# Kernel optimization log

Hardware: AMD Instinct MI355X
Metric: run time of the kernel (lower is better)

Reference implementation:

```python
import jax, jax.numpy as jnp
import numpy as np

H = 8          # num_heads
D = 256        # num_hiddens (left == right embed dim)
DH = D // H    # per-head dim
SH = 64        # num_attention_score_hiddens
B = 4
L_LEFT = 128
L_RIGHT = 256
NEG = -1e6


def _split_heads(x):
    # [B, L, D] -> [B*H, L, D/H]
    b, l, d = x.shape
    return x.reshape(b, l, H, d // H).transpose(0, 2, 1, 3).reshape(b * H, l, d // H)


def _merge_heads(x):
    # [B*H, L, dh] -> [B, L, H*dh]
    bh, l, dh = x.shape
    return x.reshape(-1, H, l, dh).transpose(0, 2, 1, 3).reshape(-1, l, H * dh)


def _additive_attention(q, k, v, valid, Wq, Wk, wv):
    # q: [BH, Lq, dh], k/v: [BH, Lk, dh], valid: [BH] int
    qf = q @ Wq                                   # [BH, Lq, SH]
    kf = k @ Wk                                   # [BH, Lk, SH]
    feats = jnp.tanh(qf[:, :, None, :] + kf[:, None, :, :])   # [BH, Lq, Lk, SH]
    scores = jnp.einsum('bqkh,h->bqk', feats, wv)              # [BH, Lq, Lk]
    lk = k.shape[1]
    mask = jnp.arange(lk)[None, None, :] < valid[:, None, None]
    scores = jnp.where(mask, scores, NEG)
    w = jax.nn.softmax(scores, axis=-1)
    return w @ v                                  # [BH, Lq, dh]


def setup_inputs() -> dict:
    key = jax.random.key(0)
    ks = jax.random.split(key, 16)
    f32 = jnp.float32
    s_w = 1.0 / np.sqrt(DH)
    s_v = 1.0 / np.sqrt(SH)
    s_o = 1.0 / np.sqrt(D)
    return {
        'queries_left': jax.random.normal(ks[0], (B, L_LEFT, D), f32),
        'keys_right':   jax.random.normal(ks[1], (B, L_RIGHT, D), f32),
        'values_right': jax.random.normal(ks[2], (B, L_RIGHT, D), f32),
        'queries_right': jax.random.normal(ks[3], (B, L_RIGHT, D), f32),
        'keys_left':    jax.random.normal(ks[4], (B, L_LEFT, D), f32),
        'values_left':  jax.random.normal(ks[5], (B, L_LEFT, D), f32),
        'Wq_l': jax.random.normal(ks[6], (DH, SH), f32) * s_w,
        'Wk_l': jax.random.normal(ks[7], (DH, SH), f32) * s_w,
        'wv_l': jax.random.normal(ks[8], (SH,), f32) * s_v,
        'Wo_l': jax.random.normal(ks[9], (D, D), f32) * s_o,
        'Wq_r': jax.random.normal(ks[10], (DH, SH), f32) * s_w,
        'Wk_r': jax.random.normal(ks[11], (DH, SH), f32) * s_w,
        'wv_r': jax.random.normal(ks[12], (SH,), f32) * s_v,
        'Wo_r': jax.random.normal(ks[13], (D, D), f32) * s_o,
        'valid_lens_right': jax.random.randint(ks[14], (B,), 1, L_RIGHT + 1).astype(jnp.int32),
        'valid_lens_left':  jax.random.randint(ks[15], (B,), 1, L_LEFT + 1).astype(jnp.int32),
    }


def reference(queries_left, keys_right, values_right, queries_right, keys_left,
              values_left, Wq_l, Wk_l, wv_l, Wo_l, Wq_r, Wk_r, wv_r, Wo_r,
              valid_lens_right, valid_lens_left):
    ql = _split_heads(queries_left)
    kr = _split_heads(keys_right)
    vr = _split_heads(values_right)
    qr = _split_heads(queries_right)
    kl = _split_heads(keys_left)
    vl = _split_heads(values_left)
    vlr = jnp.repeat(valid_lens_right, H)   # [B*H]
    vll = jnp.repeat(valid_lens_left, H)
    out_l = _additive_attention(ql, kr, vr, vlr, Wq_l, Wk_l, wv_l)
    out_r = _additive_attention(qr, kl, vl, vll, Wq_r, Wk_r, wv_r)
    out_l = _merge_heads(out_l) @ Wo_l      # [B, L_LEFT, D]
    out_r = _merge_heads(out_r) @ Wo_r      # [B, L_RIGHT, D]
    return out_l, out_r
```

## Files before the change

### kernel.cpp

```cpp
#include <hip/hip_runtime.h>
#include <math.h>


#define LOG2E 1.4426950408889634f
#define SCALE2 (2.0f * LOG2E)
#define NEGS  (-2.0f * LOG2E)

#define OFF_EQL 0
#define OFF_EKL 262144
#define OFF_EQR 786432
#define OFF_EKR 1310720
#define OFF_PL  1572864
#define OFF_PR  2621440
#define OFF_HOL 3670016
#define OFF_HOR 3801088

static __device__ __forceinline__ float fast_exp2(float x) {
#if __has_builtin(__builtin_amdgcn_exp2f)
    return __builtin_amdgcn_exp2f(x);
#else
    return exp2f(x);
#endif
}
static __device__ __forceinline__ float fast_rcp(float x) {
#if __has_builtin(__builtin_amdgcn_rcpf)
    return __builtin_amdgcn_rcpf(x);
#else
    return 1.0f / x;
#endif
}

__global__ __launch_bounds__(256) void k1_proj(
    const float* __restrict__ ql, const float* __restrict__ kr,
    const float* __restrict__ qr, const float* __restrict__ kl,
    const float* __restrict__ wql, const float* __restrict__ wkl,
    const float* __restrict__ wqr, const float* __restrict__ wkr,
    float* __restrict__ ws)
{
    __shared__ float tlds[64 * 17];
    int blk = blockIdx.x;
    const float* X; const float* W; float* out; int L; int ktype;
    if (blk < 256)       { X = ql; W = wql; out = ws + OFF_EQL; L = 128; ktype = 0; }
    else if (blk < 768)  { X = kr; W = wkl; out = ws + OFF_EKL; L = 256; ktype = 1; blk -= 256; }
    else if (blk < 1280) { X = qr; W = wqr; out = ws + OFF_EQR; L = 256; ktype = 0; blk -= 768; }
    else                 { X = kl; W = wkr; out = ws + OFF_EKR; L = 128; ktype = 1; blk -= 1280; }

    const int tiles = L >> 4;
    const int bh = blk / tiles;
    const int l0 = (blk - bh * tiles) << 4;
    const int b = bh >> 3, hd = bh & 7;
    const int t = threadIdx.x;
    const int h = t & 63, lsub = t >> 6;

    float wcol[32];
#pragma unroll
    for (int j = 0; j < 32; ++j) wcol[j] = W[j * 64 + h];

    const float* xb = X + ((b * L + l0 + lsub * 4) * 256) + hd * 32;

#pragma unroll
    for (int i = 0; i < 4; ++i) {
        const float4* xp = (const float4*)(xb + i * 256);
        float acc = 0.f;
#pragma unroll
        for (int j4 = 0; j4 < 8; ++j4) {
            float4 a = xp[j4];
            acc += a.x * wcol[4 * j4 + 0];
            acc += a.y * wcol[4 * j4 + 1];
            acc += a.z * wcol[4 * j4 + 2];
            acc += a.w * wcol[4 * j4 + 3];
        }
        const float e = fast_exp2(acc * SCALE2);
        const int lloc = lsub * 4 + i;
        if (!ktype) out[(bh * L + l0 + lloc) * 64 + h] = e;
        else        tlds[h * 17 + lloc] = e;
    }
    if (ktype) {
        __syncthreads();
        const int ll = t & 15, hq = t >> 4;
#pragma unroll
        for (int hh = 0; hh < 4; ++hh) {
            const int h2 = hq + 16 * hh;
            out[bh * (64 * L) + h2 * L + l0 + ll] = tlds[h2 * 17 + ll];
        }
    }
}

template<int LK, int LQ, int RPT, int J>
static __device__ __forceinline__ void scores_side(
    int bh, int row0,
    const float* __restrict__ eq, const float* __restrict__ ek,
    const float* __restrict__ wv, int valid, float* __restrict__ P)
{
    const int lane = threadIdx.x & 63;
    float acc[RPT][J];
#pragma unroll
    for (int r = 0; r < RPT; ++r)
#pragma unroll
        for (int j = 0; j < J; ++j) acc[r][j] = 0.f;

    const float* ekb = ek + bh * (64 * LK) + lane;
    const float* eqb = eq + (bh * LQ + row0) * 64;

#pragma unroll
    for (int j = 0; j < J; ++j) {
        if (64 * j < valid) {
#pragma unroll
            for (int hc = 0; hc < 16; ++hc) {
                const float4 wv4 = *(const float4*)(wv + hc * 4);
                float wva[4] = {wv4.x, wv4.y, wv4.z, wv4.w};
                float eqa[RPT][4];
#pragma unroll
                for (int r = 0; r < RPT; ++r) {
                    const float4 q4 = *(const float4*)(eqb + r * 64 + hc * 4);
                    eqa[r][0] = q4.x; eqa[r][1] = q4.y; eqa[r][2] = q4.z; eqa[r][3] = q4.w;
                }
#pragma unroll
                for (int hs = 0; hs < 4; ++hs) {
                    const float ekv = ekb[(hc * 4 + hs) * LK + 64 * j];
#pragma unroll
                    for (int pr = 0; pr < RPT / 2; ++pr) {
                        const float d0 = fmaf(eqa[2 * pr    ][hs], ekv, 1.0f);
                        const float d1 = fmaf(eqa[2 * pr + 1][hs], ekv, 1.0f);
                        const float rr = fast_rcp(d0 * d1);
                        acc[2 * pr    ][j] += (wva[hs] * d1) * rr;
                        acc[2 * pr + 1][j] += (wva[hs] * d0) * rr;
                    }
                }
            }
        }
    }

#pragma unroll
    for (int r = 0; r < RPT; ++r) {
        float sv[J];
        float m = -3.0e38f;
#pragma unroll
        for (int j = 0; j < J; ++j) {
            sv[j] = (64 * j + lane < valid) ? acc[r][j] * NEGS : -1.0e6f;
            m = fmaxf(m, sv[j]);
        }
#pragma unroll
        for (int off = 1; off < 64; off <<= 1) m = fmaxf(m, __shfl_xor(m, off));
        float lsum = 0.f;
#pragma unroll
        for (int j = 0; j < J; ++j) { sv[j] = fast_exp2(sv[j] - m); lsum += sv[j]; }
#pragma unroll
        for (int off = 1; off < 64; off <<= 1) lsum += __shfl_xor(lsum, off);
        const float inv = fast_rcp(lsum);
        float* pp = P + (bh * LQ + row0 + r) * LK + lane;
#pragma unroll
        for (int j = 0; j < J; ++j) pp[64 * j] = sv[j] * inv;
    }
}

__global__ __launch_bounds__(256) void k2a_scores(
    const float* __restrict__ eql, const float* __restrict__ ekl,
    const float* __restrict__ eqr, const float* __restrict__ ekr,
    const float* __restrict__ wvl, const float* __restrict__ wvr,
    const int* __restrict__ vlr, const int* __restrict__ vll,
    float* __restrict__ pl, float* __restrict__ pr)
{
    const int w = threadIdx.x >> 6;
    int blk = blockIdx.x;
    if (blk < 512) {
        const int bh = blk >> 4, q0 = (blk & 15) << 3;
        scores_side<256, 128, 2, 4>(bh, q0 + 2 * w, eql, ekl, wvl,
                                    vlr[bh >> 3], pl);
    } else {
        blk -= 512;
        const int bh = blk >> 4, q0 = (blk & 15) << 4;
        scores_side<128, 256, 4, 2>(bh, q0 + 4 * w, eqr, ekr, wvr,
                                    vll[bh >> 3], pr);
    }
}

template<int LK, int LQ>
static __device__ __forceinline__ void pv_side(
    int bh, int q0, const float* __restrict__ P,
    const float* __restrict__ v, int valid,
    float* __restrict__ ho, float* pv_lds)
{
    constexpr int TQ = 8, CS = LK / 8;
    const int t = threadIdx.x;
    const int d = t & 31, kc = t >> 5;
    const int b = bh >> 3, hd = bh & 7;

    if (kc * CS < valid) {
        float vv[CS];
        const float* vp = v + (b * LK + kc * CS) * 256 + hd * 32 + d;
#pragma unroll
        for (int i = 0; i < CS; ++i) vv[i] = vp[i * 256];
#pragma unroll
        for (int row = 0; row < TQ; ++row) {
            const float4* pp = (const float4*)(P + (bh * LQ + q0 + row) * LK + kc * CS);
            float a = 0.f;
#pragma unroll
            for (int i4 = 0; i4 < CS / 4; ++i4) {
                float4 p = pp[i4];
                a += p.x * vv[4 * i4 + 0];
                a += p.y * vv[4 * i4 + 1];
                a += p.z * vv[4 * i4 + 2];
                a += p.w * vv[4 * i4 + 3];
            }
            pv_lds[(kc * TQ + row) * 32 + d] = a;
        }
    } else {
#pragma unroll
        for (int row = 0; row < TQ; ++row) pv_lds[(kc * TQ + row) * 32 + d] = 0.f;
    }
    __syncthreads();

    const int dd = t & 31, row = t >> 5;
    float o = 0.f;
#pragma unroll
    for (int kc2 = 0; kc2 < 8; ++kc2) o += pv_lds[(kc2 * TQ + row) * 32 + dd];
    ho[(b * LQ + q0 + row) * 256 + hd * 32 + dd] = o;
}

__global__ __launch_bounds__(256) void k2b_pv(
    const float* __restrict__ pl, const float* __restrict__ pr,
    const float* __restrict__ vr, const float* __restrict__ vl,
    const int* __restrict__ vlr, const int* __restrict__ vll,
    float* __restrict__ hol, float* __restrict__ hor)
{
    __shared__ __align__(16) float pv_lds[2048];
    int blk = blockIdx.x;
    if (blk < 512) {
        const int bh = blk >> 4, q0 = (blk & 15) << 3;
        pv_side<256, 128>(bh, q0, pl, vr, vlr[bh >> 3], hol, pv_lds);
    } else {
        blk -= 512;
        const int bh = blk >> 5, q0 = (blk & 31) << 3;
        pv_side<128, 256>(bh, q0, pr, vl, vll[bh >> 3], hor, pv_lds);
    }
}

__global__ __launch_bounds__(256) void k3_proj(
    const float* __restrict__ ws,
    const float* __restrict__ wol, const float* __restrict__ wor,
    float* __restrict__ out)
{
    __shared__ __align__(16) float a_lds[1024];
    const int row0 = blockIdx.x * 4;
    const float* A; const float* W; float* op; int lr0;
    if (row0 < 512) { A = ws + OFF_HOL; W = wol; op = out;          lr0 = row0; }
    else            { A = ws + OFF_HOR; W = wor; op = out + 131072; lr0 = row0 - 512; }

    const int t = threadIdx.x;
#pragma unroll
    for (int i = 0; i < 4; ++i) a_lds[i * 256 + t] = A[(lr0 + i) * 256 + t];
    __syncthreads();

    float acc[4];
#pragma unroll
    for (int r = 0; r < 4; ++r) acc[r] = 0.f;

#pragma unroll 4
    for (int k4 = 0; k4 < 64; ++k4) {
        const float w0 = W[(k4 * 4 + 0) * 256 + t];
        const float w1 = W[(k4 * 4 + 1) * 256 + t];
        const float w2 = W[(k4 * 4 + 2) * 256 + t];
        const float w3 = W[(k4 * 4 + 3) * 256 + t];
#pragma unroll
        for (int r = 0; r < 4; ++r) {
            const float4 a = *(const float4*)(a_lds + r * 256 + k4 * 4);
            acc[r] += a.x * w0 + a.y * w1 + a.z * w2 + a.w * w3;
        }
    }
#pragma unroll
    for (int r = 0; r < 4; ++r) op[(lr0 + r) * 256 + t] = acc[r];
}

extern "C" void kernel_launch(void* const* d_in, const int* in_sizes, int n_in,
                              void* d_out, int out_size, void* d_ws, size_t ws_size,
                              hipStream_t stream)
{
    const float* ql  = (const float*)d_in[0];
    const float* kr  = (const float*)d_in[1];
    const float* vr  = (const float*)d_in[2];
    const float* qr  = (const float*)d_in[3];
    const float* kl  = (const float*)d_in[4];
    const float* vl  = (const float*)d_in[5];
    const float* wql = (const float*)d_in[6];
    const float* wkl = (const float*)d_in[7];
    const float* wvl = (const float*)d_in[8];
    const float* wol = (const float*)d_in[9];
    const float* wqr = (const float*)d_in[10];
    const float* wkr = (const float*)d_in[11];
    const float* wvr = (const float*)d_in[12];
    const float* wor = (const float*)d_in[13];
    const int*   vlr = (const int*)d_in[14];
    const int*   vll = (const int*)d_in[15];
    float* ws  = (float*)d_ws;
    float* out = (float*)d_out;

    hipLaunchKernelGGL(k1_proj, dim3(1536), dim3(256), 0, stream,
                       ql, kr, qr, kl, wql, wkl, wqr, wkr, ws);
    hipLaunchKernelGGL(k2a_scores, dim3(1024), dim3(256), 0, stream,
                       ws + OFF_EQL, ws + OFF_EKL, ws + OFF_EQR, ws + OFF_EKR,
                       wvl, wvr, vlr, vll, ws + OFF_PL, ws + OFF_PR);
    hipLaunchKernelGGL(k2b_pv, dim3(1536), dim3(256), 0, stream,
                       ws + OFF_PL, ws + OFF_PR, vr, vl, vlr, vll,
                       ws + OFF_HOL, ws + OFF_HOR);
    hipLaunchKernelGGL(k3_proj, dim3(384), dim3(256), 0, stream,
                       ws, wol, wor, out);
}
```

Before: 134.3 us.

## Fuse attention scores/softmax with PV product, keeping probabilities in LDS

Merges the scores+softmax kernel and the P·V kernel into one kernel. Softmax probabilities stay in shared memory instead of making a round trip through a global workspace (about 8 MB written and read). This also drops one kernel launch. In exchange, each block needs more LDS (24 KB), which may lower occupancy; a launch-bounds hint targets 6 waves. The PV stage now reads V again for each 8- or 16-row tile.

```diff
diff --git a/kernel.cpp b/kernel.cpp
--- a/kernel.cpp
+++ b/kernel.cpp
@@ -10,10 +10,8 @@
 #define OFF_EKL 262144
 #define OFF_EQR 786432
 #define OFF_EKR 1310720
-#define OFF_PL  1572864
-#define OFF_PR  2621440
-#define OFF_HOL 3670016
-#define OFF_HOR 3801088
+#define OFF_HOL 1572864
+#define OFF_HOR 1703936
 
 static __device__ __forceinline__ float fast_exp2(float x) {
 #if __has_builtin(__builtin_amdgcn_exp2f)
@@ -86,153 +84,145 @@
     }
 }
 
-template<int LK, int LQ, int RPT, int J>
-static __device__ __forceinline__ void scores_side(
-    int bh, int row0,
+template<int LK, int LQ, int TQ>
+static __device__ __forceinline__ void attn_fused(
+    int bh, int q0,
     const float* __restrict__ eq, const float* __restrict__ ek,
-    const float* __restrict__ wv, int valid, float* __restrict__ P)
-{
-    const int lane = threadIdx.x & 63;
-    float acc[RPT][J];
-#pragma unroll
-    for (int r = 0; r < RPT; ++r)
-#pragma unroll
-        for (int j = 0; j < J; ++j) acc[r][j] = 0.f;
-
-    const float* ekb = ek + bh * (64 * LK) + lane;
-    const float* eqb = eq + (bh * LQ + row0) * 64;
-
-#pragma unroll
-    for (int j = 0; j < J; ++j) {
-        if (64 * j < valid) {
-#pragma unroll
-            for (int hc = 0; hc < 16; ++hc) {
-                const float4 wv4 = *(const float4*)(wv + hc * 4);
-                float wva[4] = {wv4.x, wv4.y, wv4.z, wv4.w};
-                float eqa[RPT][4];
-#pragma unroll
-                for (int r = 0; r < RPT; ++r) {
-                    const float4 q4 = *(const float4*)(eqb + r * 64 + hc * 4);
-                    eqa[r][0] = q4.x; eqa[r][1] = q4.y; eqa[r][2] = q4.z; eqa[r][3] = q4.w;
-                }
-#pragma unroll
-                for (int hs = 0; hs < 4; ++hs) {
-                    const float ekv = ekb[(hc * 4 + hs) * LK + 64 * j];
-#pragma unroll
-                    for (int pr = 0; pr < RPT / 2; ++pr) {
-                        const float d0 = fmaf(eqa[2 * pr    ][hs], ekv, 1.0f);
-                        const float d1 = fmaf(eqa[2 * pr + 1][hs], ekv, 1.0f);
-                        const float rr = fast_rcp(d0 * d1);
-                        acc[2 * pr    ][j] += (wva[hs] * d1) * rr;
-                        acc[2 * pr + 1][j] += (wva[hs] * d0) * rr;
+    const float* __restrict__ wv, const float* __restrict__ v,
+    int valid, float* __restrict__ ho,
+    float* P_lds, float* pv_lds)
+{
+    constexpr int RPT = TQ / 4;
+    constexpr int J   = LK / 64;
+    constexpr int CS  = LK / 8;
+    const int t = threadIdx.x;
+    const int lane = t & 63, w = t >> 6;
+    const int b = bh >> 3, hd = bh & 7;
+
+    {
+        const int row0 = w * RPT;
+        float acc[RPT][J];
+#pragma unroll
+        for (int r = 0; r < RPT; ++r)
+#pragma unroll
+            for (int j = 0; j < J; ++j) acc[r][j] = 0.f;
+
+        const float* ekb = ek + bh * (64 * LK) + lane;
+        const float* eqb = eq + (bh * LQ + q0 + row0) * 64;
+
+#pragma unroll
+        for (int j = 0; j < J; ++j) {
+            if (64 * j < valid) {
+#pragma unroll
+                for (int hc = 0; hc < 16; ++hc) {
+                    const float4 wv4 = *(const float4*)(wv + hc * 4);
+                    float wva[4] = {wv4.x, wv4.y, wv4.z, wv4.w};
+                    float eqa[RPT][4];
+#pragma unroll
+                    for (int r = 0; r < RPT; ++r) {
+                        const float4 q4 = *(const float4*)(eqb + r * 64 + hc * 4);
+                        eqa[r][0] = q4.x; eqa[r][1] = q4.y;
+                        eqa[r][2] = q4.z; eqa[r][3] = q4.w;
+                    }
+#pragma unroll
+                    for (int hs = 0; hs < 4; ++hs) {
+                        const float ekv = ekb[(hc * 4 + hs) * LK + 64 * j];
+#pragma unroll
+                        for (int pr = 0; pr < RPT / 2; ++pr) {
+                            const float d0 = fmaf(eqa[2 * pr    ][hs], ekv, 1.0f);
+                            const float d1 = fmaf(eqa[2 * pr + 1][hs], ekv, 1.0f);
+                            const float rr = fast_rcp(d0 * d1);
+                            acc[2 * pr    ][j] += (wva[hs] * d1) * rr;
+                            acc[2 * pr + 1][j] += (wva[hs] * d0) * rr;
+                        }
                     }
                 }
             }
         }
-    }
-
-#pragma unroll
-    for (int r = 0; r < RPT; ++r) {
-        float sv[J];
-        float m = -3.0e38f;
-#pragma unroll
-        for (int j = 0; j < J; ++j) {
-            sv[j] = (64 * j + lane < valid) ? acc[r][j] * NEGS : -1.0e6f;
-            m = fmaxf(m, sv[j]);
-        }
-#pragma unroll
-        for (int off = 1; off < 64; off <<= 1) m = fmaxf(m, __shfl_xor(m, off));
-        float lsum = 0.f;
-#pragma unroll
-        for (int j = 0; j < J; ++j) { sv[j] = fast_exp2(sv[j] - m); lsum += sv[j]; }
-#pragma unroll
-        for (int off = 1; off < 64; off <<= 1) lsum += __shfl_xor(lsum, off);
-        const float inv = fast_rcp(lsum);
-        float* pp = P + (bh * LQ + row0 + r) * LK + lane;
-#pragma unroll
-        for (int j = 0; j < J; ++j) pp[64 * j] = sv[j] * inv;
-    }
-}
-
-__global__ __launch_bounds__(256) void k2a_scores(
+
+#pragma unroll
+        for (int r = 0; r < RPT; ++r) {
+            float sv[J];
+            float m = -3.0e38f;
+#pragma unroll
+            for (int j = 0; j < J; ++j) {
+                sv[j] = (64 * j + lane < valid) ? acc[r][j] * NEGS : -1.0e6f;
+                m = fmaxf(m, sv[j]);
+            }
+#pragma unroll
+            for (int off = 1; off < 64; off <<= 1) m = fmaxf(m, __shfl_xor(m, off));
+            float lsum = 0.f;
+#pragma unroll
+            for (int j = 0; j < J; ++j) { sv[j] = fast_exp2(sv[j] - m); lsum += sv[j]; }
+#pragma unroll
+            for (int off = 1; off < 64; off <<= 1) lsum += __shfl_xor(lsum, off);
+            const float inv = fast_rcp(lsum);
+#pragma unroll
+            for (int j = 0; j < J; ++j)
+                P_lds[(row0 + r) * LK + 64 * j + lane] = sv[j] * inv;
+        }
+    }
+    __syncthreads();
+
+    {
+        const int d = t & 31, kc = t >> 5;
+        float acc2[TQ];
+#pragma unroll
+        for (int row = 0; row < TQ; ++row) acc2[row] = 0.f;
+
+        if (kc * CS < valid) {
+            const float* vp = v + (b * LK + kc * CS) * 256 + hd * 32 + d;
+#pragma unroll
+            for (int c = 0; c < CS / 8; ++c) {
+                float vv[8];
+#pragma unroll
+                for (int i = 0; i < 8; ++i) vv[i] = vp[(c * 8 + i) * 256];
+#pragma unroll
+                for (int row = 0; row < TQ; ++row) {
+                    const float4* pp = (const float4*)(P_lds + row * LK + kc * CS + c * 8);
+                    const float4 p0 = pp[0], p1 = pp[1];
+                    acc2[row] += p0.x * vv[0] + p0.y * vv[1] + p0.z * vv[2] + p0.w * vv[3]
+                               + p1.x * vv[4] + p1.y * vv[5] + p1.z * vv[6] + p1.w * vv[7];
+                }
+            }
+        }
+#pragma unroll
+        for (int row = 0; row < TQ; ++row)
+            pv_lds[(kc * TQ + row) * 32 + d] = acc2[row];
+    }
+    __syncthreads();
+
+#pragma unroll
+    for (int rr = 0; rr < (TQ * 32) / 256; ++rr) {
+        const int idx = t + 256 * rr;
+        const int dd = idx & 31, row = idx >> 5;
+        float o = 0.f;
+#pragma unroll
+        for (int kc2 = 0; kc2 < 8; ++kc2) o += pv_lds[(kc2 * TQ + row) * 32 + dd];
+        ho[(b * LQ + q0 + row) * 256 + hd * 32 + dd] = o;
+    }
+}
+
+__global__ __launch_bounds__(256, 6) void k2_attn(
     const float* __restrict__ eql, const float* __restrict__ ekl,
     const float* __restrict__ eqr, const float* __restrict__ ekr,
     const float* __restrict__ wvl, const float* __restrict__ wvr,
+    const float* __restrict__ vr, const float* __restrict__ vl,
     const int* __restrict__ vlr, const int* __restrict__ vll,
-    float* __restrict__ pl, float* __restrict__ pr)
-{
-    const int w = threadIdx.x >> 6;
+    float* __restrict__ hol, float* __restrict__ hor)
+{
+    __shared__ __align__(16) float P_lds[2048];
+    __shared__ __align__(16) float pv_lds[4096];
     int blk = blockIdx.x;
     if (blk < 512) {
         const int bh = blk >> 4, q0 = (blk & 15) << 3;
-        scores_side<256, 128, 2, 4>(bh, q0 + 2 * w, eql, ekl, wvl,
-                                    vlr[bh >> 3], pl);
+        attn_fused<256, 128, 8>(bh, q0, eql, ekl, wvl, vr, vlr[bh >> 3],
+                                hol, P_lds, pv_lds);
     } else {
         blk -= 512;
         const int bh = blk >> 4, q0 = (blk & 15) << 4;
-        scores_side<128, 256, 4, 2>(bh, q0 + 4 * w, eqr, ekr, wvr,
-                                    vll[bh >> 3], pr);
-    }
-}
-
-template<int LK, int LQ>
-static __device__ __forceinline__ void pv_side(
-    int bh, int q0, const float* __restrict__ P,
-    const float* __restrict__ v, int valid,
-    float* __restrict__ ho, float* pv_lds)
-{
-    constexpr int TQ = 8, CS = LK / 8;
-    const int t = threadIdx.x;
-    const int d = t & 31, kc = t >> 5;
-    const int b = bh >> 3, hd = bh & 7;
-
-    if (kc * CS < valid) {
-        float vv[CS];
-        const float* vp = v + (b * LK + kc * CS) * 256 + hd * 32 + d;
-#pragma unroll
-        for (int i = 0; i < CS; ++i) vv[i] = vp[i * 256];
-#pragma unroll
-        for (int row = 0; row < TQ; ++row) {
-            const float4* pp = (const float4*)(P + (bh * LQ + q0 + row) * LK + kc * CS);
-            float a = 0.f;
-#pragma unroll
-            for (int i4 = 0; i4 < CS / 4; ++i4) {
-                float4 p = pp[i4];
-                a += p.x * vv[4 * i4 + 0];
-                a += p.y * vv[4 * i4 + 1];
-                a += p.z * vv[4 * i4 + 2];
-                a += p.w * vv[4 * i4 + 3];
-            }
-            pv_lds[(kc * TQ + row) * 32 + d] = a;
-        }
-    } else {
-#pragma unroll
-        for (int row = 0; row < TQ; ++row) pv_lds[(kc * TQ + row) * 32 + d] = 0.f;
-    }
-    __syncthreads();
-
-    const int dd = t & 31, row = t >> 5;
-    float o = 0.f;
-#pragma unroll
-    for (int kc2 = 0; kc2 < 8; ++kc2) o += pv_lds[(kc2 * TQ + row) * 32 + dd];
-    ho[(b * LQ + q0 + row) * 256 + hd * 32 + dd] = o;
-}
-
-__global__ __launch_bounds__(256) void k2b_pv(
-    const float* __restrict__ pl, const float* __restrict__ pr,
-    const float* __restrict__ vr, const float* __restrict__ vl,
-    const int* __restrict__ vlr, const int* __restrict__ vll,
-    float* __restrict__ hol, float* __restrict__ hor)
-{
-    __shared__ __align__(16) float pv_lds[2048];
-    int blk = blockIdx.x;
-    if (blk < 512) {
-        const int bh = blk >> 4, q0 = (blk & 15) << 3;
-        pv_side<256, 128>(bh, q0, pl, vr, vlr[bh >> 3], hol, pv_lds);
-    } else {
-        blk -= 512;
-        const int bh = blk >> 5, q0 = (blk & 31) << 3;
-        pv_side<128, 256>(bh, q0, pr, vl, vll[bh >> 3], hor, pv_lds);
+        attn_fused<128, 256, 16>(bh, q0, eqr, ekr, wvr, vl, vll[bh >> 3],
+                                 hor, P_lds, pv_lds);
     }
 }
 
@@ -297,11 +287,9 @@
 
     hipLaunchKernelGGL(k1_proj, dim3(1536), dim3(256), 0, stream,
                        ql, kr, qr, kl, wql, wkl, wqr, wkr, ws);
-    hipLaunchKernelGGL(k2a_scores, dim3(1024), dim3(256), 0, stream,
+    hipLaunchKernelGGL(k2_attn, dim3(1024), dim3(256), 0, stream,
                        ws + OFF_EQL, ws + OFF_EKL, ws + OFF_EQR, ws + OFF_EKR,
-                       wvl, wvr, vlr, vll, ws + OFF_PL, ws + OFF_PR);
-    hipLaunchKernelGGL(k2b_pv, dim3(1536), dim3(256), 0, stream,
-                       ws + OFF_PL, ws + OFF_PR, vr, vl, vlr, vll,
+                       wvl, wvr, vr, vl, vlr, vll,
                        ws + OFF_HOL, ws + OFF_HOR);
     hipLaunchKernelGGL(k3_proj, dim3(384), dim3(256), 0, stream,
                        ws, wol, wor, out);
```

After: 131.9 us (median of 2 runs). No clear change (-1.7%).
